# Kernel tuning notes

Hardware: AMD Instinct MI355X
Metric: run time of the kernel (lower is better)

The kernel has to match this reference:

```python
import jax, jax.numpy as jnp
import numpy as np
import math

B, S, E, H, DK = 2, 2048, 1024, 16, 64  # batch, seq, embed, heads, d_k (= n_wires)

def setup_inputs() -> dict:
    key = jax.random.key(0)
    k1, k2, k3, k4, k5 = jax.random.split(key, 5)
    scale = 0.02
    return {
        "x": jax.random.normal(k1, (B, S, E), dtype=jnp.float32),
        "Wk": jax.random.normal(k2, (E, E), dtype=jnp.float32) * scale,
        "Wv": jax.random.normal(k3, (E, E), dtype=jnp.float32) * scale,
        "Wq": jax.random.normal(k4, (H, DK, E), dtype=jnp.float32) * scale,
        "theta": jax.random.normal(k5, (DK,), dtype=jnp.float32) * scale,
    }

def reference(x, Wk, Wv, Wq, theta):
    batch, seq, embed = x.shape
    n_heads, d_k = Wq.shape[0], Wq.shape[1]
    # K, V projections (nn.Linear, no bias): x @ W.T
    k = (x @ Wk.T).reshape(batch, seq, n_heads, d_k).transpose(0, 2, 1, 3)  # [B,H,S,dk]
    v = (x @ Wv.T).reshape(batch, seq, n_heads, d_k).transpose(0, 2, 1, 3)  # [B,H,S,dk]
    # Quantum query path: per-head linear proj -> RX(proj_i) then RX(theta_i) on wire i from |0>,
    # MeasureAll(PauliZ) on independent wires gives <Z_i> = cos(proj_i + theta_i) exactly.
    proj = jnp.einsum('bse,hde->bhsd', x, Wq)          # [B,H,S,dk]
    q = jnp.cos(proj + theta)                           # [B,H,S,dk]
    scores = jnp.einsum('bhsd,bhtd->bhst', q, k) / math.sqrt(d_k)  # [B,H,S,S]
    attn = jax.nn.softmax(scores, axis=-1)
    out = jnp.einsum('bhst,bhtd->bhsd', attn, v)        # [B,H,S,dk]
    return out.transpose(0, 2, 1, 3).reshape(batch, seq, embed)
```

## Files before the change

kernel.cpp:

```cpp
#include <hip/hip_runtime.h>
#include <hip/hip_bf16.h>

constexpr int B  = 2;
constexpr int S  = 2048;
constexpr int E  = 1024;
constexpr int H  = 16;
constexpr int DK = 64;
constexpr int M  = B * S;
constexpr int N3 = 3 * E;
constexpr long RSZ = (long)B * H * S * DK;

using bf16x8 = __attribute__((ext_vector_type(8))) __bf16;
using bf16x4 = __attribute__((ext_vector_type(4))) __bf16;
using f32x4  = __attribute__((ext_vector_type(4))) float;

__device__ __forceinline__ void async16(__bf16* lds, const __bf16* g) {
    __builtin_amdgcn_global_load_lds(
        (const __attribute__((address_space(1))) void*)g,
        (__attribute__((address_space(3))) void*)lds, 16, 0, 0);
}

__global__ __launch_bounds__(256)
void cvt_kernel(const float* __restrict__ x, const float* __restrict__ Wk,
                const float* __restrict__ Wv, const float* __restrict__ Wq,
                __bf16* __restrict__ xb, __bf16* __restrict__ wall) {
    const long e = ((long)blockIdx.x * 256 + threadIdx.x) * 4;
    const float* src;
    __bf16* dst;
    if (e < (long)M * E) { src = x + e; dst = xb + e; }
    else {
        const long e2 = e - (long)M * E;
        const int which = (int)(e2 >> 20);
        const long off  = e2 & ((1L << 20) - 1);
        src = (which == 0 ? Wk : which == 1 ? Wv : Wq) + off;
        dst = wall + e2;
    }
    float4 f = *reinterpret_cast<const float4*>(src);
    bf16x4 o;
    o[0] = (__bf16)f.x; o[1] = (__bf16)f.y; o[2] = (__bf16)f.z; o[3] = (__bf16)f.w;
    *reinterpret_cast<bf16x4*>(dst) = o;
}

__global__ __launch_bounds__(256, 3)
void qkv_gemm(const __bf16* __restrict__ xb, const __bf16* __restrict__ wall,
              const float* __restrict__ theta, __bf16* __restrict__ kvq) {
    __shared__ __align__(1024) __bf16 smem[4 * 128 * 32];
    __bf16* tile = smem;

    const int t    = threadIdx.x;
    const int lane = t & 63;
    const int w    = t >> 6;
    const int quad = lane >> 4;
    const int l16  = lane & 15;
    const int wm   = w >> 1, wn = w & 1;
    const int mbase = blockIdx.y * 128;
    const int nbase = blockIdx.x * 128;

    f32x4 acc[4][4];
    #pragma unroll
    for (int i = 0; i < 4; i++)
        #pragma unroll
        for (int j = 0; j < 4; j++)
            acc[i][j] = f32x4{0.f, 0.f, 0.f, 0.f};

    const int srow = lane >> 2;
    const int srcc = (lane & 3) ^ ((lane >> 3) & 3);
    const __bf16* ga = xb   + (long)(mbase + srow) * E + srcc * 8;
    const __bf16* gb = wall + (long)(nbase + srow) * E + srcc * 8;

    const int csw = (l16 >> 1) & 3;

    #pragma unroll
    for (int c = 0; c < 2; c++) {
        async16(smem +        (c * 64 + w * 16) * 32, ga + (long)(c * 64 + w * 16) * E);
        async16(smem + 8192 + (c * 64 + w * 16) * 32, gb + (long)(c * 64 + w * 16) * E);
    }

    for (int it = 0; it < E / 32; it++) {
        const int cur = it & 1;
        __syncthreads();

        if (it + 1 < E / 32) {
            const int kk1 = (it + 1) * 32;
            #pragma unroll
            for (int c = 0; c < 2; c++) {
                async16(smem + (cur ^ 1) * 4096 +        (c * 64 + w * 16) * 32,
                        ga + (long)(c * 64 + w * 16) * E + kk1);
                async16(smem + (cur ^ 1) * 4096 + 8192 + (c * 64 + w * 16) * 32,
                        gb + (long)(c * 64 + w * 16) * E + kk1);
            }
        }

        const __bf16* Asb = smem + cur * 4096;
        const __bf16* Bsb = smem + cur * 4096 + 8192;
        bf16x8 a[4], b[4];
        #pragma unroll
        for (int i = 0; i < 4; i++)
            a[i] = *reinterpret_cast<const bf16x8*>(
                &Asb[(wm * 64 + i * 16 + l16) * 32 + (quad ^ csw) * 8]);
        #pragma unroll
        for (int j = 0; j < 4; j++)
            b[j] = *reinterpret_cast<const bf16x8*>(
                &Bsb[(wn * 64 + j * 16 + l16) * 32 + (quad ^ csw) * 8]);
        #pragma unroll
        for (int i = 0; i < 4; i++)
            #pragma unroll
            for (int j = 0; j < 4; j++)
                acc[i][j] = __builtin_amdgcn_mfma_f32_16x16x32_bf16(a[i], b[j], acc[i][j], 0, 0, 0);
    }

    const int region = nbase >> 10;
    const int bb = mbase >> 11;
    if (region == 1) {
        __syncthreads();
        #pragma unroll
        for (int i = 0; i < 4; i++) {
            const int cchunk = wm * 8 + i * 2 + (quad >> 1);
            #pragma unroll
            for (int j = 0; j < 4; j++) {
                const int cirb = wn * 64 + j * 16 + l16;
                const int cs = cchunk ^ l16;
                bf16x4 pk;
                #pragma unroll
                for (int r = 0; r < 4; r++) pk[r] = (__bf16)acc[i][j][r];
                *reinterpret_cast<bf16x4*>(&tile[cirb * 128 + cs * 8 + (quad & 1) * 4]) = pk;
            }
        }
        __syncthreads();
        const int h0 = (nbase & 1023) >> 6;
        __bf16* vt = kvq + RSZ;
        #pragma unroll
        for (int p = 0; p < 8; p++) {
            const int dcol = p * 16 + (t >> 4);
            const int lc = t & 15;
            const int cs2 = lc ^ (dcol & 15);
            bf16x8 vv = *reinterpret_cast<const bf16x8*>(&tile[dcol * 128 + cs2 * 8]);
            const int hh = h0 + (dcol >> 6), d = dcol & 63;
            *reinterpret_cast<bf16x8*>(
                &vt[((long)(bb * H + hh) * DK + d) * S + (mbase & 2047) + lc * 8]) = vv;
        }
    } else {
        __bf16* dst = kvq + (region == 2 ? 2 * RSZ : 0);
        float th[4];
        if (region == 2) {
            #pragma unroll
            for (int j = 0; j < 4; j++) th[j] = theta[j * 16 + l16];
        }
        #pragma unroll
        for (int i = 0; i < 4; i++) {
            const int row0 = mbase + wm * 64 + i * 16 + quad * 4;
            #pragma unroll
            for (int j = 0; j < 4; j++) {
                const int cir = (nbase & 1023) + wn * 64 + j * 16 + l16;
                const int h = cir >> 6, d = cir & 63;
                #pragma unroll
                for (int r = 0; r < 4; r++) {
                    const int s = (row0 + r) & 2047;
                    float v = acc[i][j][r];
                    if (region == 2) v = cosf(v + th[j]) * 0.125f;
                    dst[((long)(bb * H + h) * S + s) * DK + d] = (__bf16)v;
                }
            }
        }
    }
}

__global__ __launch_bounds__(256, 3)
void attn_kernel(const __bf16* __restrict__ q_ws, const __bf16* __restrict__ k_ws,
                 const __bf16* __restrict__ v_ws, float* __restrict__ out) {
    __shared__ __align__(1024) __bf16 Ks[2][64 * 64];
    __shared__ __align__(1024) __bf16 Vs[2][64 * 64];
    __shared__ __align__(16)   __bf16 p_c[4][2048];

    const int lane = threadIdx.x & 63;
    const int w    = threadIdx.x >> 6;
    const int quad = lane >> 4;
    const int l16  = lane & 15;
    const int bh    = blockIdx.y;
    const int qbase = blockIdx.x * 128 + w * 32;

    const __bf16* qp = q_ws + (long)bh * S * DK;
    const __bf16* kp = k_ws + (long)bh * S * DK;
    const __bf16* vp = v_ws + (long)bh * DK * S;

    const int sr  = lane >> 3;
    const int sc  = lane & 7;
    const int scs = sc ^ sr;

    bf16x8 aq[2][2];
    #pragma unroll
    for (int mt = 0; mt < 2; mt++)
        #pragma unroll
        for (int ks = 0; ks < 2; ks++)
            aq[mt][ks] = *reinterpret_cast<const bf16x8*>(
                qp + (long)(qbase + mt * 16 + l16) * DK + ks * 32 + quad * 8);

    bf16x8 vone;
    #pragma unroll
    for (int j = 0; j < 8; j++) vone[j] = (__bf16)1.0f;

    f32x4 o[2][4];
    #pragma unroll
    for (int i = 0; i < 2; i++)
        #pragma unroll
        for (int j = 0; j < 4; j++) o[i][j] = f32x4{0.f, 0.f, 0.f, 0.f};
    f32x4 ls[2] = {f32x4{0.f, 0.f, 0.f, 0.f}, f32x4{0.f, 0.f, 0.f, 0.f}};

    const int prd = (l16 & 3) * 256 + (quad >> 1) * 64 + (l16 >> 2) * 16 + (quad & 1) * 8;

    #pragma unroll
    for (int i = 0; i < 2; i++) {
        const int row = i * 32 + w * 8;
        async16(&Ks[0][row * 64], kp + (long)(row + sr) * DK + scs * 8);
        async16(&Vs[0][row * 64], vp + (long)(row + sr) * S + scs * 8);
    }

    for (int it = 0; it < S / 64; it++) {
        const int cur = it & 1;
        __syncthreads();

        if (it + 1 < S / 64) {
            const int kt1 = (it + 1) * 64;
            #pragma unroll
            for (int i = 0; i < 2; i++) {
                const int row = i * 32 + w * 8;
                async16(&Ks[cur ^ 1][row * 64], kp + (long)(kt1 + row + sr) * DK + scs * 8);
                async16(&Vs[cur ^ 1][row * 64], vp + (long)(row + sr) * S + kt1 + scs * 8);
            }
        }

        f32x4 sacc[2][4];
        #pragma unroll
        for (int i = 0; i < 2; i++)
            #pragma unroll
            for (int j = 0; j < 4; j++) sacc[i][j] = f32x4{0.f, 0.f, 0.f, 0.f};
        #pragma unroll
        for (int ks = 0; ks < 2; ks++) {
            bf16x8 bk[4];
            #pragma unroll
            for (int nt = 0; nt < 4; nt++)
                bk[nt] = *reinterpret_cast<const bf16x8*>(
                    &Ks[cur][(nt * 16 + l16) * 64 + ((ks * 4 + quad) ^ (l16 & 7)) * 8]);
            #pragma unroll
            for (int mt = 0; mt < 2; mt++)
                #pragma unroll
                for (int nt = 0; nt < 4; nt++)
                    sacc[mt][nt] = __builtin_amdgcn_mfma_f32_16x16x32_bf16(
                        aq[mt][ks], bk[nt], sacc[mt][nt], 0, 0, 0);
        }
        #pragma unroll
        for (int mt = 0; mt < 2; mt++)
            #pragma unroll
            for (int r = 0; r < 4; r++)
                #pragma unroll
                for (int nt = 0; nt < 4; nt++)
                    p_c[w][((mt * 4 + r) * 4 + nt) * 64 + lane] =
                        (__bf16)__expf(sacc[mt][nt][r]);
        #pragma unroll
        for (int ks = 0; ks < 2; ks++) {
            bf16x8 ap[2];
            #pragma unroll
            for (int mt = 0; mt < 2; mt++)
                ap[mt] = *reinterpret_cast<const bf16x8*>(
                    &p_c[w][prd + mt * 1024 + ks * 128]);
            bf16x8 bv[4];
            #pragma unroll
            for (int nd = 0; nd < 4; nd++)
                bv[nd] = *reinterpret_cast<const bf16x8*>(
                    &Vs[cur][(nd * 16 + l16) * 64 + ((ks * 4 + quad) ^ (l16 & 7)) * 8]);
            #pragma unroll
            for (int mt = 0; mt < 2; mt++) {
                ls[mt] = __builtin_amdgcn_mfma_f32_16x16x32_bf16(ap[mt], vone, ls[mt], 0, 0, 0);
                #pragma unroll
                for (int nd = 0; nd < 4; nd++)
                    o[mt][nd] = __builtin_amdgcn_mfma_f32_16x16x32_bf16(
                        ap[mt], bv[nd], o[mt][nd], 0, 0, 0);
            }
        }
    }

    const int b = bh >> 4, h = bh & 15;
    #pragma unroll
    for (int mt = 0; mt < 2; mt++) {
        #pragma unroll
        for (int r = 0; r < 4; r++) {
            const float inv = 1.0f / ls[mt][r];
            const int srow = qbase + mt * 16 + quad * 4 + r;
            #pragma unroll
            for (int nd = 0; nd < 4; nd++)
                out[(long)(b * S + srow) * E + h * DK + nd * 16 + l16] = o[mt][nd][r] * inv;
        }
    }
}

__device__ inline bf16x8 cvt_frag(const float* __restrict__ p) {
    float4 f0 = *reinterpret_cast<const float4*>(p);
    float4 f1 = *reinterpret_cast<const float4*>(p + 4);
    bf16x8 r;
    r[0] = (__bf16)f0.x; r[1] = (__bf16)f0.y; r[2] = (__bf16)f0.z; r[3] = (__bf16)f0.w;
    r[4] = (__bf16)f1.x; r[5] = (__bf16)f1.y; r[6] = (__bf16)f1.z; r[7] = (__bf16)f1.w;
    return r;
}
template <int MODE>
__global__ __launch_bounds__(256, 2)
void proj_kernel(const float* __restrict__ x, const float* __restrict__ W,
                 const float* __restrict__ theta, __bf16* __restrict__ out) {
    const int lane = threadIdx.x & 63;
    const int w    = threadIdx.x >> 6;
    const int quad = lane >> 4;
    const int l16  = lane & 15;
    const int mbase = blockIdx.y * 128 + w * 32;
    const int nbase = blockIdx.x * 128;
    f32x4 acc[2][8];
    #pragma unroll
    for (int i = 0; i < 2; i++)
        #pragma unroll
        for (int j = 0; j < 8; j++) acc[i][j] = f32x4{0.f, 0.f, 0.f, 0.f};
    float th[4];
    if (MODE == 2) {
        #pragma unroll
        for (int j = 0; j < 4; j++) th[j] = theta[j * 16 + l16];
    }
    for (int kk = 0; kk < E; kk += 32) {
        bf16x8 a[2], b[8];
        #pragma unroll
        for (int mt = 0; mt < 2; mt++)
            a[mt] = cvt_frag(x + (long)(mbase + mt * 16 + l16) * E + kk + quad * 8);
        #pragma unroll
        for (int nt = 0; nt < 8; nt++)
            b[nt] = cvt_frag(W + (long)(nbase + nt * 16 + l16) * E + kk + quad * 8);
        #pragma unroll
        for (int mt = 0; mt < 2; mt++)
            #pragma unroll
            for (int nt = 0; nt < 8; nt++)
                acc[mt][nt] = __builtin_amdgcn_mfma_f32_16x16x32_bf16(a[mt], b[nt], acc[mt][nt], 0, 0, 0);
    }
    #pragma unroll
    for (int mt = 0; mt < 2; mt++) {
        const int row0 = mbase + mt * 16 + quad * 4;
        #pragma unroll
        for (int nt = 0; nt < 8; nt++) {
            const int col = nbase + nt * 16 + l16;
            const int h = col >> 6, d = col & 63;
            #pragma unroll
            for (int r = 0; r < 4; r++) {
                const int row = row0 + r;
                const int bb = row >> 11, s = row & 2047;
                float v = acc[mt][nt][r];
                if (MODE == 2) v = cosf(v + th[nt & 3]) * 0.125f;
                long idx;
                if (MODE == 1) idx = ((long)(bb * H + h) * DK + d) * S + s;
                else           idx = ((long)(bb * H + h) * S + s) * DK + d;
                out[idx] = (__bf16)v;
            }
        }
    }
}

extern "C" void kernel_launch(void* const* d_in, const int* in_sizes, int n_in,
                              void* d_out, int out_size, void* d_ws, size_t ws_size,
                              hipStream_t stream) {
    const float* x     = (const float*)d_in[0];
    const float* Wk    = (const float*)d_in[1];
    const float* Wv    = (const float*)d_in[2];
    const float* Wq    = (const float*)d_in[3];
    const float* theta = (const float*)d_in[4];
    float* out = (float*)d_out;

    __bf16* kvq  = (__bf16*)d_ws;
    __bf16* xb   = kvq + 3 * RSZ;
    __bf16* wall = xb + (long)M * E;
    __bf16* k_ws = kvq;
    __bf16* v_t  = kvq + RSZ;
    __bf16* q_ws = kvq + 2 * RSZ;

    const size_t need = (3 * RSZ + (long)M * E + (long)N3 * E) * 2;
    dim3 blk(256);
    if (ws_size >= need) {
        cvt_kernel<<<dim3(7168), blk, 0, stream>>>(x, Wk, Wv, Wq, xb, wall);
        qkv_gemm<<<dim3(N3 / 128, M / 128), blk, 0, stream>>>(xb, wall, theta, kvq);
    } else {
        dim3 gp(E / 128, M / 128);
        proj_kernel<0><<<gp, blk, 0, stream>>>(x, Wk, nullptr, k_ws);
        proj_kernel<1><<<gp, blk, 0, stream>>>(x, Wv, nullptr, v_t);
        proj_kernel<2><<<gp, blk, 0, stream>>>(x, Wq, theta, q_ws);
    }

    attn_kernel<<<dim3(S / 128, B * H), blk, 0, stream>>>(q_ws, k_ws, v_t, out);
}
```

Measured before the change: 186.0 us.

## Shrink attention tiles to 16 query rows per wave and 32-key blocks

Restructures the attention kernel so each wave handles 16 query rows instead of 32 and each iteration loads a 32-key tile instead of 64. The grid grows from 512 to 1024 blocks, uses a 1D grid with a bh-interleaved block mapping, and raises the occupancy target to 4 blocks per CU with smaller LDS and register use. It also replaces the P staging buffer with a padded 16x40 layout. The aim is more parallelism and latency hiding, at the cost of half the K/V reuse per load, twice as many loop iterations and barriers, and less MFMA work per synchronisation.

```diff
diff --git a/kernel.cpp b/kernel.cpp
--- a/kernel.cpp
+++ b/kernel.cpp
@@ -165,19 +165,21 @@
     }
 }
 
-__global__ __launch_bounds__(256, 3)
+__global__ __launch_bounds__(256, 4)
 void attn_kernel(const __bf16* __restrict__ q_ws, const __bf16* __restrict__ k_ws,
                  const __bf16* __restrict__ v_ws, float* __restrict__ out) {
-    __shared__ __align__(1024) __bf16 Ks[2][64 * 64];
-    __shared__ __align__(1024) __bf16 Vs[2][64 * 64];
-    __shared__ __align__(16)   __bf16 p_c[4][2048];
+    __shared__ __align__(1024) __bf16 Ks[2][32 * 64];
+    __shared__ __align__(1024) __bf16 Vs[2][64 * 32];
+    __shared__ __align__(16)   __bf16 p_lds[4][16][40];
 
     const int lane = threadIdx.x & 63;
     const int w    = threadIdx.x >> 6;
     const int quad = lane >> 4;
     const int l16  = lane & 15;
-    const int bh    = blockIdx.y;
-    const int qbase = blockIdx.x * 128 + w * 32;
+
+    const int id    = blockIdx.x;
+    const int bh    = (id & 7) + 8 * ((id >> 3) & 3);
+    const int qbase = (id >> 5) * 64 + w * 16;
 
     const __bf16* qp = q_ws + (long)bh * S * DK;
     const __bf16* kp = k_ws + (long)bh * S * DK;
@@ -186,110 +188,75 @@
     const int sr  = lane >> 3;
     const int sc  = lane & 7;
     const int scs = sc ^ sr;
-
-    bf16x8 aq[2][2];
-    #pragma unroll
-    for (int mt = 0; mt < 2; mt++)
-        #pragma unroll
-        for (int ks = 0; ks < 2; ks++)
-            aq[mt][ks] = *reinterpret_cast<const bf16x8*>(
-                qp + (long)(qbase + mt * 16 + l16) * DK + ks * 32 + quad * 8);
+    const int vr  = lane >> 2;
+    const int vc  = lane & 3;
+    const int vcs = vc ^ (vr & 3);
+
+    bf16x8 aq[2];
+    #pragma unroll
+    for (int ks = 0; ks < 2; ks++)
+        aq[ks] = *reinterpret_cast<const bf16x8*>(
+            qp + (long)(qbase + l16) * DK + ks * 32 + quad * 8);
 
     bf16x8 vone;
     #pragma unroll
     for (int j = 0; j < 8; j++) vone[j] = (__bf16)1.0f;
 
-    f32x4 o[2][4];
-    #pragma unroll
-    for (int i = 0; i < 2; i++)
-        #pragma unroll
-        for (int j = 0; j < 4; j++) o[i][j] = f32x4{0.f, 0.f, 0.f, 0.f};
-    f32x4 ls[2] = {f32x4{0.f, 0.f, 0.f, 0.f}, f32x4{0.f, 0.f, 0.f, 0.f}};
-
-    const int prd = (l16 & 3) * 256 + (quad >> 1) * 64 + (l16 >> 2) * 16 + (quad & 1) * 8;
-
-    #pragma unroll
-    for (int i = 0; i < 2; i++) {
-        const int row = i * 32 + w * 8;
-        async16(&Ks[0][row * 64], kp + (long)(row + sr) * DK + scs * 8);
-        async16(&Vs[0][row * 64], vp + (long)(row + sr) * S + scs * 8);
-    }
-
-    for (int it = 0; it < S / 64; it++) {
+    f32x4 o[4];
+    #pragma unroll
+    for (int j = 0; j < 4; j++) o[j] = f32x4{0.f, 0.f, 0.f, 0.f};
+    f32x4 ls = f32x4{0.f, 0.f, 0.f, 0.f};
+
+    async16(&Ks[0][(w * 8) * 64], kp + (long)(w * 8 + sr) * DK + scs * 8);
+    async16(&Vs[0][(w * 16) * 32], vp + (long)(w * 16 + vr) * S + vcs * 8);
+
+    for (int it = 0; it < S / 32; it++) {
         const int cur = it & 1;
         __syncthreads();
 
-        if (it + 1 < S / 64) {
-            const int kt1 = (it + 1) * 64;
-            #pragma unroll
-            for (int i = 0; i < 2; i++) {
-                const int row = i * 32 + w * 8;
-                async16(&Ks[cur ^ 1][row * 64], kp + (long)(kt1 + row + sr) * DK + scs * 8);
-                async16(&Vs[cur ^ 1][row * 64], vp + (long)(row + sr) * S + kt1 + scs * 8);
-            }
-        }
-
-        f32x4 sacc[2][4];
-        #pragma unroll
-        for (int i = 0; i < 2; i++)
-            #pragma unroll
-            for (int j = 0; j < 4; j++) sacc[i][j] = f32x4{0.f, 0.f, 0.f, 0.f};
+        if (it + 1 < S / 32) {
+            const int kt1 = (it + 1) * 32;
+            async16(&Ks[cur ^ 1][(w * 8) * 64],
+                    kp + (long)(kt1 + w * 8 + sr) * DK + scs * 8);
+            async16(&Vs[cur ^ 1][(w * 16) * 32],
+                    vp + (long)(w * 16 + vr) * S + kt1 + vcs * 8);
+        }
+
+        f32x4 sacc[2];
+        sacc[0] = f32x4{0.f, 0.f, 0.f, 0.f};
+        sacc[1] = f32x4{0.f, 0.f, 0.f, 0.f};
         #pragma unroll
         for (int ks = 0; ks < 2; ks++) {
-            bf16x8 bk[4];
-            #pragma unroll
-            for (int nt = 0; nt < 4; nt++)
-                bk[nt] = *reinterpret_cast<const bf16x8*>(
+            #pragma unroll
+            for (int nt = 0; nt < 2; nt++) {
+                bf16x8 bk = *reinterpret_cast<const bf16x8*>(
                     &Ks[cur][(nt * 16 + l16) * 64 + ((ks * 4 + quad) ^ (l16 & 7)) * 8]);
-            #pragma unroll
-            for (int mt = 0; mt < 2; mt++)
-                #pragma unroll
-                for (int nt = 0; nt < 4; nt++)
-                    sacc[mt][nt] = __builtin_amdgcn_mfma_f32_16x16x32_bf16(
-                        aq[mt][ks], bk[nt], sacc[mt][nt], 0, 0, 0);
-        }
-        #pragma unroll
-        for (int mt = 0; mt < 2; mt++)
+                sacc[nt] = __builtin_amdgcn_mfma_f32_16x16x32_bf16(aq[ks], bk, sacc[nt], 0, 0, 0);
+            }
+        }
+        #pragma unroll
+        for (int nt = 0; nt < 2; nt++)
             #pragma unroll
             for (int r = 0; r < 4; r++)
-                #pragma unroll
-                for (int nt = 0; nt < 4; nt++)
-                    p_c[w][((mt * 4 + r) * 4 + nt) * 64 + lane] =
-                        (__bf16)__expf(sacc[mt][nt][r]);
-        #pragma unroll
-        for (int ks = 0; ks < 2; ks++) {
-            bf16x8 ap[2];
-            #pragma unroll
-            for (int mt = 0; mt < 2; mt++)
-                ap[mt] = *reinterpret_cast<const bf16x8*>(
-                    &p_c[w][prd + mt * 1024 + ks * 128]);
-            bf16x8 bv[4];
-            #pragma unroll
-            for (int nd = 0; nd < 4; nd++)
-                bv[nd] = *reinterpret_cast<const bf16x8*>(
-                    &Vs[cur][(nd * 16 + l16) * 64 + ((ks * 4 + quad) ^ (l16 & 7)) * 8]);
-            #pragma unroll
-            for (int mt = 0; mt < 2; mt++) {
-                ls[mt] = __builtin_amdgcn_mfma_f32_16x16x32_bf16(ap[mt], vone, ls[mt], 0, 0, 0);
-                #pragma unroll
-                for (int nd = 0; nd < 4; nd++)
-                    o[mt][nd] = __builtin_amdgcn_mfma_f32_16x16x32_bf16(
-                        ap[mt], bv[nd], o[mt][nd], 0, 0, 0);
-            }
+                p_lds[w][quad * 4 + r][nt * 16 + l16] = (__bf16)__expf(sacc[nt][r]);
+        bf16x8 ap = *reinterpret_cast<const bf16x8*>(&p_lds[w][l16][quad * 8]);
+        ls = __builtin_amdgcn_mfma_f32_16x16x32_bf16(ap, vone, ls, 0, 0, 0);
+        #pragma unroll
+        for (int nd = 0; nd < 4; nd++) {
+            bf16x8 bv = *reinterpret_cast<const bf16x8*>(
+                &Vs[cur][(nd * 16 + l16) * 32 + (quad ^ (l16 & 3)) * 8]);
+            o[nd] = __builtin_amdgcn_mfma_f32_16x16x32_bf16(ap, bv, o[nd], 0, 0, 0);
         }
     }
 
     const int b = bh >> 4, h = bh & 15;
     #pragma unroll
-    for (int mt = 0; mt < 2; mt++) {
-        #pragma unroll
-        for (int r = 0; r < 4; r++) {
-            const float inv = 1.0f / ls[mt][r];
-            const int srow = qbase + mt * 16 + quad * 4 + r;
-            #pragma unroll
-            for (int nd = 0; nd < 4; nd++)
-                out[(long)(b * S + srow) * E + h * DK + nd * 16 + l16] = o[mt][nd][r] * inv;
-        }
+    for (int r = 0; r < 4; r++) {
+        const float inv = 1.0f / ls[r];
+        const int srow = qbase + quad * 4 + r;
+        #pragma unroll
+        for (int nd = 0; nd < 4; nd++)
+            out[(long)(b * S + srow) * E + h * DK + nd * 16 + l16] = o[nd][r] * inv;
     }
 }
 
@@ -386,5 +353,5 @@
         proj_kernel<2><<<gp, blk, 0, stream>>>(x, Wq, theta, q_ws);
     }
 
-    attn_kernel<<<dim3(S / 128, B * H), blk, 0, stream>>>(q_ws, k_ws, v_t, out);
-}
+    attn_kernel<<<dim3(1024), blk, 0, stream>>>(q_ws, k_ws, v_t, out);
+}
```

Result: faster. 180.1 us (-3.2%).

## Restructure attention to transposed S=K·Q tiles with 2-wave blocks and 32-key steps

Applied to the files above, without the earlier changes.

Rewrites the attention kernel so each wave handles 64 queries with Q held as the B operand and K as the A operand, computing transposed score tiles. Key and value tiles step by 32 keys instead of 64. Row sums move from an MFMA against a ones vector to VALU accumulation with a shuffle reduction, and P is staged through padded LDS. Blocks shrink to 128 threads, and a 1D grid of 512 blocks is remapped so consecutive blocks cover different heads. The aim is to cut MFMA work and LDS traffic per key, at the cost of twice as many barriers per key and lower occupancy from launch_bounds(128,1).

```diff
diff --git a/kernel.cpp b/kernel.cpp
--- a/kernel.cpp
+++ b/kernel.cpp
@@ -165,67 +165,63 @@
     }
 }
 
-__global__ __launch_bounds__(256, 3)
+__global__ __launch_bounds__(128, 1)
 void attn_kernel(const __bf16* __restrict__ q_ws, const __bf16* __restrict__ k_ws,
                  const __bf16* __restrict__ v_ws, float* __restrict__ out) {
-    __shared__ __align__(1024) __bf16 Ks[2][64 * 64];
-    __shared__ __align__(1024) __bf16 Vs[2][64 * 64];
-    __shared__ __align__(16)   __bf16 p_c[4][2048];
+    __shared__ __align__(1024) __bf16 Ks[2][32 * 64];
+    __shared__ __align__(1024) __bf16 Vs[2][64 * 32];
+    __shared__ __align__(16)   __bf16 Pl[2][64 * 40];
+    __shared__ __align__(16)   float  ls_lds[2][64];
 
     const int lane = threadIdx.x & 63;
     const int w    = threadIdx.x >> 6;
     const int quad = lane >> 4;
     const int l16  = lane & 15;
-    const int bh    = blockIdx.y;
-    const int qbase = blockIdx.x * 128 + w * 32;
+
+    const int id    = blockIdx.x;
+    const int bh    = (id & 7) + 8 * ((id >> 3) & 3);
+    const int qbase = (id >> 5) * 128 + w * 64;
 
     const __bf16* qp = q_ws + (long)bh * S * DK;
     const __bf16* kp = k_ws + (long)bh * S * DK;
     const __bf16* vp = v_ws + (long)bh * DK * S;
 
-    const int sr  = lane >> 3;
-    const int sc  = lane & 7;
-    const int scs = sc ^ sr;
-
-    bf16x8 aq[2][2];
-    #pragma unroll
-    for (int mt = 0; mt < 2; mt++)
+    const int ksr = lane >> 3, ksc = (lane & 7) ^ (lane >> 3);
+    const int vsr = lane >> 2, vsc = (lane & 3) ^ ((lane >> 2) & 3);
+
+    bf16x8 bq[4][2];
+    #pragma unroll
+    for (int nt = 0; nt < 4; nt++)
         #pragma unroll
         for (int ks = 0; ks < 2; ks++)
-            aq[mt][ks] = *reinterpret_cast<const bf16x8*>(
-                qp + (long)(qbase + mt * 16 + l16) * DK + ks * 32 + quad * 8);
-
-    bf16x8 vone;
-    #pragma unroll
-    for (int j = 0; j < 8; j++) vone[j] = (__bf16)1.0f;
-
-    f32x4 o[2][4];
-    #pragma unroll
-    for (int i = 0; i < 2; i++)
+            bq[nt][ks] = *reinterpret_cast<const bf16x8*>(
+                qp + (long)(qbase + nt * 16 + l16) * DK + ks * 32 + quad * 8);
+
+    f32x4 o[4][4];
+    #pragma unroll
+    for (int i = 0; i < 4; i++)
         #pragma unroll
         for (int j = 0; j < 4; j++) o[i][j] = f32x4{0.f, 0.f, 0.f, 0.f};
-    f32x4 ls[2] = {f32x4{0.f, 0.f, 0.f, 0.f}, f32x4{0.f, 0.f, 0.f, 0.f}};
-
-    const int prd = (l16 & 3) * 256 + (quad >> 1) * 64 + (l16 >> 2) * 16 + (quad & 1) * 8;
+    float lsum[4] = {0.f, 0.f, 0.f, 0.f};
 
     #pragma unroll
     for (int i = 0; i < 2; i++) {
-        const int row = i * 32 + w * 8;
-        async16(&Ks[0][row * 64], kp + (long)(row + sr) * DK + scs * 8);
-        async16(&Vs[0][row * 64], vp + (long)(row + sr) * S + scs * 8);
-    }
-
-    for (int it = 0; it < S / 64; it++) {
+        async16(&Ks[0][(w * 16 + i * 8) * 64], kp + (long)(w * 16 + i * 8 + ksr) * DK + ksc * 8);
+        async16(&Vs[0][(w * 32 + i * 16) * 32], vp + (long)(w * 32 + i * 16 + vsr) * S + vsc * 8);
+    }
+
+    for (int it = 0; it < S / 32; it++) {
         const int cur = it & 1;
         __syncthreads();
 
-        if (it + 1 < S / 64) {
-            const int kt1 = (it + 1) * 64;
+        if (it + 1 < S / 32) {
+            const int kt1 = (it + 1) * 32;
             #pragma unroll
             for (int i = 0; i < 2; i++) {
-                const int row = i * 32 + w * 8;
-                async16(&Ks[cur ^ 1][row * 64], kp + (long)(kt1 + row + sr) * DK + scs * 8);
-                async16(&Vs[cur ^ 1][row * 64], vp + (long)(row + sr) * S + kt1 + scs * 8);
+                async16(&Ks[cur ^ 1][(w * 16 + i * 8) * 64],
+                        kp + (long)(kt1 + w * 16 + i * 8 + ksr) * DK + ksc * 8);
+                async16(&Vs[cur ^ 1][(w * 32 + i * 16) * 32],
+                        vp + (long)(w * 32 + i * 16 + vsr) * S + kt1 + vsc * 8);
             }
         }
 
@@ -236,59 +232,67 @@
             for (int j = 0; j < 4; j++) sacc[i][j] = f32x4{0.f, 0.f, 0.f, 0.f};
         #pragma unroll
         for (int ks = 0; ks < 2; ks++) {
-            bf16x8 bk[4];
-            #pragma unroll
-            for (int nt = 0; nt < 4; nt++)
-                bk[nt] = *reinterpret_cast<const bf16x8*>(
-                    &Ks[cur][(nt * 16 + l16) * 64 + ((ks * 4 + quad) ^ (l16 & 7)) * 8]);
+            bf16x8 ak[2];
+            #pragma unroll
+            for (int mt = 0; mt < 2; mt++)
+                ak[mt] = *reinterpret_cast<const bf16x8*>(
+                    &Ks[cur][(mt * 16 + l16) * 64 + ((ks * 4 + quad) ^ (l16 & 7)) * 8]);
             #pragma unroll
             for (int mt = 0; mt < 2; mt++)
                 #pragma unroll
                 for (int nt = 0; nt < 4; nt++)
                     sacc[mt][nt] = __builtin_amdgcn_mfma_f32_16x16x32_bf16(
-                        aq[mt][ks], bk[nt], sacc[mt][nt], 0, 0, 0);
-        }
+                        ak[mt], bq[nt][ks], sacc[mt][nt], 0, 0, 0);
+        }
+
         #pragma unroll
         for (int mt = 0; mt < 2; mt++)
             #pragma unroll
-            for (int r = 0; r < 4; r++)
-                #pragma unroll
-                for (int nt = 0; nt < 4; nt++)
-                    p_c[w][((mt * 4 + r) * 4 + nt) * 64 + lane] =
-                        (__bf16)__expf(sacc[mt][nt][r]);
-        #pragma unroll
-        for (int ks = 0; ks < 2; ks++) {
-            bf16x8 ap[2];
-            #pragma unroll
-            for (int mt = 0; mt < 2; mt++)
-                ap[mt] = *reinterpret_cast<const bf16x8*>(
-                    &p_c[w][prd + mt * 1024 + ks * 128]);
-            bf16x8 bv[4];
-            #pragma unroll
-            for (int nd = 0; nd < 4; nd++)
-                bv[nd] = *reinterpret_cast<const bf16x8*>(
-                    &Vs[cur][(nd * 16 + l16) * 64 + ((ks * 4 + quad) ^ (l16 & 7)) * 8]);
-            #pragma unroll
-            for (int mt = 0; mt < 2; mt++) {
-                ls[mt] = __builtin_amdgcn_mfma_f32_16x16x32_bf16(ap[mt], vone, ls[mt], 0, 0, 0);
-                #pragma unroll
-                for (int nd = 0; nd < 4; nd++)
-                    o[mt][nd] = __builtin_amdgcn_mfma_f32_16x16x32_bf16(
-                        ap[mt], bv[nd], o[mt][nd], 0, 0, 0);
-            }
-        }
+            for (int nt = 0; nt < 4; nt++) {
+                float p0 = __expf(sacc[mt][nt][0]);
+                float p1 = __expf(sacc[mt][nt][1]);
+                float p2 = __expf(sacc[mt][nt][2]);
+                float p3 = __expf(sacc[mt][nt][3]);
+                lsum[nt] += (p0 + p1) + (p2 + p3);
+                bf16x4 pk;
+                pk[0] = (__bf16)p0; pk[1] = (__bf16)p1;
+                pk[2] = (__bf16)p2; pk[3] = (__bf16)p3;
+                *reinterpret_cast<bf16x4*>(
+                    &Pl[w][(nt * 16 + l16) * 40 + mt * 16 + quad * 4]) = pk;
+            }
+
+        #pragma unroll
+        for (int mt = 0; mt < 4; mt++) {
+            bf16x8 ap = *reinterpret_cast<const bf16x8*>(
+                &Pl[w][(mt * 16 + l16) * 40 + quad * 8]);
+            #pragma unroll
+            for (int nt = 0; nt < 4; nt++) {
+                bf16x8 bv = *reinterpret_cast<const bf16x8*>(
+                    &Vs[cur][(nt * 16 + l16) * 32 + (quad ^ (l16 & 3)) * 8]);
+                o[mt][nt] = __builtin_amdgcn_mfma_f32_16x16x32_bf16(ap, bv, o[mt][nt], 0, 0, 0);
+            }
+        }
+    }
+
+    #pragma unroll
+    for (int nt = 0; nt < 4; nt++) {
+        float v = lsum[nt];
+        v += __shfl_xor(v, 16);
+        v += __shfl_xor(v, 32);
+        ls_lds[w][nt * 16 + l16] = v;
     }
 
     const int b = bh >> 4, h = bh & 15;
     #pragma unroll
-    for (int mt = 0; mt < 2; mt++) {
+    for (int mt = 0; mt < 4; mt++) {
+        f32x4 lv = *reinterpret_cast<const f32x4*>(&ls_lds[w][mt * 16 + quad * 4]);
         #pragma unroll
         for (int r = 0; r < 4; r++) {
-            const float inv = 1.0f / ls[mt][r];
+            const float inv = 1.0f / lv[r];
             const int srow = qbase + mt * 16 + quad * 4 + r;
             #pragma unroll
-            for (int nd = 0; nd < 4; nd++)
-                out[(long)(b * S + srow) * E + h * DK + nd * 16 + l16] = o[mt][nd][r] * inv;
+            for (int nt = 0; nt < 4; nt++)
+                out[(long)(b * S + srow) * E + h * DK + nt * 16 + l16] = o[mt][nt][r] * inv;
         }
     }
 }
@@ -386,5 +390,5 @@
         proj_kernel<2><<<gp, blk, 0, stream>>>(x, Wq, theta, q_ws);
     }
 
-    attn_kernel<<<dim3(S / 128, B * H), blk, 0, stream>>>(q_ws, k_ws, v_t, out);
-}
+    attn_kernel<<<dim3(512), dim3(128), 0, stream>>>(q_ws, k_ws, v_t, out);
+}
```

Result: slower. 219.9 us (+18.3%).
